# Kernel tuning notes

Hardware: AMD Instinct MI355X
Metric: run time of the kernel (lower is better)

The kernel has to match this reference:

```python
import jax, jax.numpy as jnp
import numpy as np

DIM = 256; QK = 256; HEADS = 8; TOPK = 2; WV = 2; WH = 2
SCALE = QK ** -0.5


def setup_inputs() -> dict:
    key = jax.random.key(0)
    ks = jax.random.split(key, 6)
    x = jax.random.normal(ks[0], (4, DIM, 64, 64), jnp.float32)
    Wqkv = jax.random.normal(ks[1], (DIM, 2 * QK + DIM), jnp.float32) * 0.02
    bqkv = jnp.zeros((2 * QK + DIM,), jnp.float32)
    Wo = jax.random.normal(ks[2], (DIM, DIM), jnp.float32) * 0.02
    bo = jnp.zeros((DIM,), jnp.float32)
    lepe_w = jax.random.normal(ks[3], (3, 3, 1, DIM), jnp.float32) * 0.1  # HWIO depthwise
    lepe_b = jnp.zeros((DIM,), jnp.float32)
    return {"x": x, "Wqkv": Wqkv, "bqkv": bqkv, "Wo": Wo, "bo": bo,
            "lepe_w": lepe_w, "lepe_b": lepe_b}


def _dwconv(x, w, b):
    # depthwise 3x3 conv, NHWC
    y = jax.lax.conv_general_dilated(x, w, (1, 1), 'SAME',
                                     dimension_numbers=('NHWC', 'HWIO', 'NHWC'),
                                     feature_group_count=x.shape[-1])
    return y + b


def _branch(win, Wqkv, bqkv, lepe_w, lepe_b, to_image):
    n, p2, h, w, _ = win.shape
    w2 = h * w
    qkv = win @ Wqkv + bqkv
    q = qkv[..., :QK]
    kv = qkv[..., QK:]                                  # [n,p2,h,w,QK+DIM]
    q_pix = q.reshape(n, p2, w2, QK)
    kv_pix = kv.reshape(n, p2, w2, QK + DIM)            # identity kv_down
    # region routing (detached in original)
    q_win = jax.lax.stop_gradient(q).mean((2, 3))       # [n,p2,QK]
    k_win = jax.lax.stop_gradient(kv[..., :QK]).mean((2, 3))
    logit = jnp.einsum('npc,nqc->npq', q_win * SCALE, k_win)
    _, r_idx = jax.lax.top_k(logit, TOPK)               # [n,p2,TOPK]
    # gather selected KV windows (mul_weight='none')
    kv_sel = jax.vmap(lambda kvb, idxb: kvb[idxb])(kv_pix, r_idx)  # [n,p2,k,w2,ckv]
    k_sel = kv_sel[..., :QK].reshape(n, p2, TOPK * w2, HEADS, QK // HEADS)
    v_sel = kv_sel[..., QK:].reshape(n, p2, TOPK * w2, HEADS, DIM // HEADS)
    qh = q_pix.reshape(n, p2, w2, HEADS, QK // HEADS)
    attn = jax.nn.softmax(jnp.einsum('npqhd,npkhd->nphqk', qh * SCALE, k_sel), axis=-1)
    out = jnp.einsum('nphqk,npkhd->npqhd', attn, v_sel).reshape(n, p2, h, w, DIM)
    lepe = _dwconv(to_image(kv[..., QK:]), lepe_w, lepe_b)
    return to_image(out) + lepe


def reference(x, Wqkv, bqkv, Wo, bo, lepe_w, lepe_b):
    xh = x.transpose(0, 2, 3, 1)                        # NHWC
    N, H, W, C = xh.shape
    v_win, h_win = H // WV, W // WH
    # vertical branch: horizontal strips of height WV, full width
    vm = xh.reshape(N, v_win, WV, W, C)
    # horizontal branch: vertical strips of width WH, full height
    hm = xh.reshape(N, H, h_win, WH, C).transpose(0, 2, 1, 3, 4)
    img_v = lambda a: a.reshape(N, H, W, a.shape[-1])
    img_h = lambda a: a.transpose(0, 2, 1, 3, 4).reshape(N, H, W, a.shape[-1])
    o1 = _branch(vm, Wqkv, bqkv, lepe_w, lepe_b, img_v)
    o2 = _branch(hm, Wqkv, bqkv, lepe_w, lepe_b, img_h)
    out = (o1 @ Wo + bo) + (o2 @ Wo + bo)
    return out.transpose(0, 3, 1, 2)                    # back to NCHW
```

## Files before the change

kernel.cpp:

```cpp
#include <hip/hip_runtime.h>
#include <hip/hip_bf16.h>
#include <math.h>

#define NBATCH 4
#define HW     4096
#define NPIX   16384
#define SCALE  0.0625f
#define QLOG2E (0.0625f * 1.44269504088896340736f)

typedef __attribute__((ext_vector_type(8))) short bf16x8;
typedef __attribute__((ext_vector_type(4))) float f32x4;

__device__ __forceinline__ int pixmap(int b, int n, int p, int pos){
  return (b == 0) ? (n*HW + p*128 + pos)
                  : (n*HW + (pos >> 1)*64 + (p << 1) + (pos & 1));
}

__device__ __forceinline__ ushort f2b(float x){
  __hip_bfloat16 h = __float2bfloat16(x);
  return *reinterpret_cast<ushort*>(&h);
}
__device__ __forceinline__ float b2f(ushort u){
  __hip_bfloat16 h = *reinterpret_cast<__hip_bfloat16*>(&u);
  return __bfloat162float(h);
}
__device__ __forceinline__ uint pk2t(float a, float b){
  return (__float_as_uint(a) >> 16) | (__float_as_uint(b) & 0xFFFF0000u);
}

__global__ __launch_bounds__(256) void k_xt(
    const float* __restrict__ x, ushort* __restrict__ Xb,
    float* __restrict__ pb0, float* __restrict__ pb1)
{
  __shared__ float T[32][257];
  const int n = blockIdx.y, blk = blockIdx.x, hw0 = blk * 32;
  const int tid = threadIdx.x;
  const int hl = tid & 31, cg = tid >> 5;
  #pragma unroll 8
  for(int i = 0; i < 32; i++){
    const int c = i*8 + cg;
    T[hl][c] = x[((size_t)(n*256 + c))*4096 + hw0 + hl];
  }
  __syncthreads();
  const int c0 = (tid & 31)*8, pbr = tid >> 5;
  #pragma unroll
  for(int i = 0; i < 4; i++){
    const int p = pbr + 8*i;
    union { bf16x8 v; ushort u[8]; } U;
    #pragma unroll
    for(int j = 0; j < 8; j++) U.u[j] = f2b(T[p][c0 + j]);
    *(bf16x8*)(Xb + ((size_t)(n*HW + hw0 + p))*256 + c0) = U.v;
  }
  const int c = tid;
  float s0 = 0.f;
  float* p1 = pb1 + (((size_t)n*128 + blk)*16)*256 + c;
  #pragma unroll
  for(int j = 0; j < 16; j++){
    const float pj = T[2*j][c] + T[2*j+1][c];
    p1[(size_t)j*256] = pj;
    s0 += pj;
  }
  pb0[((size_t)n*128 + blk)*256 + c] = s0;
}

__global__ __launch_bounds__(256) void k_xred(
    const float* __restrict__ pb0, const float* __restrict__ pb1,
    float* __restrict__ xwin)
{
  const int p = blockIdx.x;
  const int n = blockIdx.y;
  const int c = threadIdx.x;
  float s = 0.f;
  #pragma unroll
  for(int i = 0; i < 4; i++)
    s += pb0[((size_t)n*128 + 4*p + i)*256 + c];
  xwin[((size_t)((0*NBATCH + n)*32 + p))*256 + c] = s * (1.f/128.f);
  const int half = p >> 4, j = p & 15;
  float s1 = 0.f;
  for(int h = 0; h < 64; h++)
    s1 += pb1[(((size_t)n*128 + 2*h + half)*16 + j)*256 + c];
  xwin[((size_t)((1*NBATCH + n)*32 + p))*256 + c] = s1 * (1.f/128.f);
}

__global__ __launch_bounds__(256) void k_wprep(
    const float* __restrict__ Wqkv, const float* __restrict__ Wo,
    ushort* __restrict__ Wt, ushort* __restrict__ WoT)
{
  const int o = blockIdx.x, t = threadIdx.x;
  if(o < 768){
    Wt[(size_t)o*256 + t] = f2b(Wqkv[(size_t)t*768 + o]);
  } else {
    const int c = o - 768;
    WoT[(size_t)c*256 + t] = f2b(Wo[(size_t)t*256 + c]);
  }
}

__global__ __launch_bounds__(256) void k_qkv_mfma(
    const ushort* __restrict__ Xb, const ushort* __restrict__ Wt,
    const float* __restrict__ bqkv, ushort* __restrict__ QKVb,
    ushort* __restrict__ Vt)
{
  const int tid = threadIdx.x;
  const int l = tid & 63, w = tid >> 6;
  const int wr = w >> 1, wc = w & 1;
  const int q16 = l & 15, g = l >> 4;
  const int row0 = blockIdx.x*128 + wr*64;
  const int col0 = blockIdx.y*128 + wc*64;

  f32x4 acc[4][4];
  #pragma unroll
  for(int i = 0; i < 4; i++)
    #pragma unroll
    for(int j = 0; j < 4; j++) acc[i][j] = (f32x4){0,0,0,0};

  const ushort* Ab = Xb + (size_t)(row0 + q16)*256 + 8*g;
  const ushort* Bb = Wt + (size_t)(col0 + q16)*256 + 8*g;

  #pragma unroll
  for(int ks = 0; ks < 8; ks++){
    const int k0 = ks*32;
    bf16x8 a[4], b[4];
    #pragma unroll
    for(int i = 0; i < 4; i++) a[i] = *(const bf16x8*)(Ab + (size_t)(16*i)*256 + k0);
    #pragma unroll
    for(int j = 0; j < 4; j++) b[j] = *(const bf16x8*)(Bb + (size_t)(16*j)*256 + k0);
    #pragma unroll
    for(int i = 0; i < 4; i++)
      #pragma unroll
      for(int j = 0; j < 4; j++)
        acc[i][j] = __builtin_amdgcn_mfma_f32_16x16x32_bf16(a[i], b[j], acc[i][j], 0, 0, 0);
  }

  const int n = row0 >> 12, hwb = row0 & 4095;
  #pragma unroll
  for(int j = 0; j < 4; j++){
    const int col = col0 + 16*j + q16;
    const float bias = bqkv[col];
    const float sc = (col < 256) ? QLOG2E : 1.f;
    #pragma unroll
    for(int i = 0; i < 4; i++){
      ushort4 u;
      u.x = f2b((acc[i][j][0] + bias) * sc);
      u.y = f2b((acc[i][j][1] + bias) * sc);
      u.z = f2b((acc[i][j][2] + bias) * sc);
      u.w = f2b((acc[i][j][3] + bias) * sc);
      const int row = row0 + 16*i + 4*g;
      QKVb[(size_t)(row+0)*768 + col] = u.x;
      QKVb[(size_t)(row+1)*768 + col] = u.y;
      QKVb[(size_t)(row+2)*768 + col] = u.z;
      QKVb[(size_t)(row+3)*768 + col] = u.w;
      if(col >= 512){
        *(ushort4*)&Vt[((size_t)(n*256 + col - 512))*4096 + hwb + 16*i + 4*g] = u;
      }
    }
  }
}

__global__ __launch_bounds__(256) void k_win_gemm(
    const float* __restrict__ xwin, const float* __restrict__ Wqkv,
    const float* __restrict__ bqkv, float* __restrict__ qwin, float* __restrict__ kwin)
{
  __shared__ float xs[256];
  const int row = blockIdx.x;
  const int tid = threadIdx.x;
  xs[tid] = xwin[(size_t)row*256 + tid];
  __syncthreads();
  #pragma unroll
  for(int half = 0; half < 2; half++){
    const int col = half*256 + tid;
    float s = 0.f;
    for(int k = 0; k < 256; k++) s += xs[k] * Wqkv[(size_t)k*768 + col];
    s += bqkv[col];
    if(half == 0) qwin[(size_t)row*256 + tid] = s;
    else          kwin[(size_t)row*256 + tid] = s;
  }
}

__global__ __launch_bounds__(256) void k_logits_top2(
    const float* __restrict__ qwin, const float* __restrict__ kwin, int* __restrict__ ridx)
{
  const int n = blockIdx.x, b = blockIdx.y;
  __shared__ float lg[32][32];
  const int base = ((b*NBATCH + n)*32)*256;
  for(int t = threadIdx.x; t < 1024; t += 256){
    const int p = t >> 5, q = t & 31;
    const float* qp = qwin + base + p*256;
    const float* kq = kwin + base + q*256;
    float s = 0.f;
    for(int c = 0; c < 256; c++) s += qp[c]*kq[c];
    lg[p][q] = s * SCALE;
  }
  __syncthreads();
  if(threadIdx.x < 32){
    const int p = threadIdx.x;
    float m0 = -INFINITY; int i0 = 0;
    for(int q = 0; q < 32; q++){ const float v = lg[p][q]; if(v > m0){ m0 = v; i0 = q; } }
    float m1 = -INFINITY; int i1 = 0;
    for(int q = 0; q < 32; q++){ if(q == i0) continue; const float v = lg[p][q]; if(v > m1){ m1 = v; i1 = q; } }
    const int o = ((b*NBATCH + n)*32 + p)*2;
    ridx[o] = i0; ridx[o+1] = i1;
  }
}

struct KVFrag { bf16x8 kf0, kf1, vf0, vf1; };

__device__ __forceinline__ KVFrag load_kv(
    const ushort* __restrict__ QKVb, const ushort* __restrict__ Vt,
    int b, int n, int wsel, int posb, int hd, int q16, int g)
{
  KVFrag f;
  const int kp0 = pixmap(b, n, wsel, posb + q16);
  f.kf0 = *(const bf16x8*)(QKVb + (size_t)kp0*768 + 256 + hd*32 + 8*g);
  const int kp1 = pixmap(b, n, wsel, posb + 16 + q16);
  f.kf1 = *(const bf16x8*)(QKVb + (size_t)kp1*768 + 256 + hd*32 + 8*g);
  if(b == 0){
    const ushort* base = Vt + ((size_t)(n*256 + hd*32 + q16))*4096 + wsel*128 + posb + 4*g;
    union { bf16x8 v; ushort4 h[2]; } U0, U1;
    U0.h[0] = *(const ushort4*)(base);
    U0.h[1] = *(const ushort4*)(base + 16);
    U1.h[0] = *(const ushort4*)(base + (size_t)16*4096);
    U1.h[1] = *(const ushort4*)(base + (size_t)16*4096 + 16);
    f.vf0 = U0.v; f.vf1 = U1.v;
  } else {
    const int h0 = (posb + 4*g) >> 1;
    const ushort* base = Vt + ((size_t)(n*256 + hd*32 + q16))*4096 + 2*wsel;
    union { bf16x8 v; uint u[4]; } U0, U1;
    U0.u[0] = *(const uint*)(base + (h0    )*64);
    U0.u[1] = *(const uint*)(base + (h0 + 1)*64);
    U0.u[2] = *(const uint*)(base + (h0 + 8)*64);
    U0.u[3] = *(const uint*)(base + (h0 + 9)*64);
    const ushort* base1 = base + (size_t)16*4096;
    U1.u[0] = *(const uint*)(base1 + (h0    )*64);
    U1.u[1] = *(const uint*)(base1 + (h0 + 1)*64);
    U1.u[2] = *(const uint*)(base1 + (h0 + 8)*64);
    U1.u[3] = *(const uint*)(base1 + (h0 + 9)*64);
    f.vf0 = U0.v; f.vf1 = U1.v;
  }
  return f;
}

__global__ __launch_bounds__(256) void k_attn_mfma(
    const ushort* __restrict__ QKVb, const ushort* __restrict__ Vt,
    const int* __restrict__ ridx, ushort* __restrict__ Ob)
{
  int id = blockIdx.x*4 + (threadIdx.x >> 6);
  const int hd = id & 7;  id >>= 3;
  const int p  = id & 31; id >>= 5;
  const int n  = id & 3;  id >>= 2;
  const int b  = id;
  const int l = threadIdx.x & 63;
  const int q16 = l & 15, g = l >> 4;

  const int ro = ((b*NBATCH + n)*32 + p)*2;
  const int r0 = ridx[ro], r1 = ridx[ro+1];

  int qpix[8];
  bf16x8 qf[8];
  #pragma unroll
  for(int m = 0; m < 8; m++){
    qpix[m] = pixmap(b, n, p, m*16 + q16);
    qf[m] = *(const bf16x8*)(QKVb + (size_t)qpix[m]*768 + hd*32 + 8*g);
  }

  f32x4 acc0[8], acc1[8];
  float rs[8];
  #pragma unroll
  for(int m = 0; m < 8; m++){
    acc0[m] = (f32x4){0,0,0,0}; acc1[m] = (f32x4){0,0,0,0}; rs[m] = 0.f;
  }

  #define COMPUTE(F)                                                            \
    __builtin_amdgcn_s_setprio(1);                                              \
    _Pragma("unroll")                                                           \
    for(int m = 0; m < 8; m++){                                                 \
      const f32x4 z = {0,0,0,0};                                                \
      f32x4 s0 = __builtin_amdgcn_mfma_f32_16x16x32_bf16((F).kf0, qf[m], z, 0, 0, 0); \
      f32x4 s1 = __builtin_amdgcn_mfma_f32_16x16x32_bf16((F).kf1, qf[m], z, 0, 0, 0); \
      const float e00 = exp2f(s0[0]), e01 = exp2f(s0[1]), e02 = exp2f(s0[2]), e03 = exp2f(s0[3]); \
      const float e10 = exp2f(s1[0]), e11 = exp2f(s1[1]), e12 = exp2f(s1[2]), e13 = exp2f(s1[3]); \
      rs[m] += ((e00+e01)+(e02+e03)) + ((e10+e11)+(e12+e13));                   \
      union { bf16x8 v; uint u[4]; } P;                                         \
      P.u[0] = pk2t(e00, e01);                                                  \
      P.u[1] = pk2t(e02, e03);                                                  \
      P.u[2] = pk2t(e10, e11);                                                  \
      P.u[3] = pk2t(e12, e13);                                                  \
      acc0[m] = __builtin_amdgcn_mfma_f32_16x16x32_bf16((F).vf0, P.v, acc0[m], 0, 0, 0); \
      acc1[m] = __builtin_amdgcn_mfma_f32_16x16x32_bf16((F).vf1, P.v, acc1[m], 0, 0, 0); \
    }                                                                           \
    __builtin_amdgcn_s_setprio(0);

  KVFrag fA = load_kv(QKVb, Vt, b, n, r0, 0, hd, q16, g);
  for(int cc = 0; cc < 8; cc += 2){
    const int w1 = (cc+1 < 4) ? r0 : r1;
    KVFrag fB = load_kv(QKVb, Vt, b, n, w1, (32*(cc+1)) & 127, hd, q16, g);
    COMPUTE(fA);
    if(cc + 2 < 8){
      const int w2 = (cc+2 < 4) ? r0 : r1;
      fA = load_kv(QKVb, Vt, b, n, w2, (32*(cc+2)) & 127, hd, q16, g);
    }
    COMPUTE(fB);
  }
  #undef COMPUTE

  #pragma unroll
  for(int m = 0; m < 8; m++){
    float r = rs[m];
    r += __shfl_xor(r, 16);
    r += __shfl_xor(r, 32);
    rs[m] = 1.f / r;
  }
  #pragma unroll
  for(int m = 0; m < 8; m++){
    ushort* op = Ob + ((size_t)b*NPIX + qpix[m])*256 + hd*32 + 4*g;
    const float iv = rs[m];
    ushort4 o0 = { f2b(acc0[m][0]*iv), f2b(acc0[m][1]*iv), f2b(acc0[m][2]*iv), f2b(acc0[m][3]*iv) };
    ushort4 o1 = { f2b(acc1[m][0]*iv), f2b(acc1[m][1]*iv), f2b(acc1[m][2]*iv), f2b(acc1[m][3]*iv) };
    *(ushort4*)op = o0;
    *(ushort4*)(op + 16) = o1;
  }
}

__global__ __launch_bounds__(256) void k_combine_lepe(
    const ushort* __restrict__ QKVb, const ushort* __restrict__ Ob0,
    const ushort* __restrict__ Ob1,
    const float* __restrict__ lw, const float* __restrict__ lb, ushort* __restrict__ Sb)
{
  const int pix = blockIdx.x;
  const int c = threadIdx.x;
  const int n = pix >> 12, rem = pix & 4095;
  const int h = rem >> 6, w = rem & 63;
  float conv = 0.f;
  #pragma unroll
  for(int kh = 0; kh < 3; kh++){
    const int hh = h + kh - 1;
    if(hh < 0 || hh >= 64) continue;
    #pragma unroll
    for(int kw = 0; kw < 3; kw++){
      const int wi = w + kw - 1;
      if(wi < 0 || wi >= 64) continue;
      const int np = (n*64 + hh)*64 + wi;
      conv += b2f(QKVb[(size_t)np*768 + 512 + c]) * lw[(kh*3 + kw)*256 + c];
    }
  }
  const size_t idx = (size_t)pix*256 + c;
  Sb[idx] = f2b(b2f(Ob0[idx]) + b2f(Ob1[idx]) + 2.f*(conv + lb[c]));
}

__global__ __launch_bounds__(256) void k_out_mfma(
    const ushort* __restrict__ Sb, const ushort* __restrict__ WoT,
    const float* __restrict__ bo, float* __restrict__ out)
{
  const int tid = threadIdx.x;
  const int l = tid & 63, w = tid >> 6;
  const int wr = w >> 1, wc = w & 1;
  const int q16 = l & 15, g = l >> 4;
  const int c0   = blockIdx.x*128 + wr*64;
  const int pix0 = blockIdx.y*128 + wc*64;
  const int n = pix0 >> 12, rem0 = pix0 & 4095;

  f32x4 acc[4][4];
  #pragma unroll
  for(int i = 0; i < 4; i++)
    #pragma unroll
    for(int j = 0; j < 4; j++) acc[i][j] = (f32x4){0,0,0,0};

  const ushort* Ab = WoT + (size_t)(c0 + q16)*256 + 8*g;
  const ushort* Bb = Sb  + (size_t)(pix0 + q16)*256 + 8*g;

  #pragma unroll
  for(int ks = 0; ks < 8; ks++){
    const int k0 = ks*32;
    bf16x8 a[4], b[4];
    #pragma unroll
    for(int i = 0; i < 4; i++) a[i] = *(const bf16x8*)(Ab + (size_t)(16*i)*256 + k0);
    #pragma unroll
    for(int j = 0; j < 4; j++) b[j] = *(const bf16x8*)(Bb + (size_t)(16*j)*256 + k0);
    #pragma unroll
    for(int i = 0; i < 4; i++)
      #pragma unroll
      for(int j = 0; j < 4; j++)
        acc[i][j] = __builtin_amdgcn_mfma_f32_16x16x32_bf16(a[i], b[j], acc[i][j], 0, 0, 0);
  }

  float* outn = out + (size_t)n*256*4096;
  #pragma unroll
  for(int i = 0; i < 4; i++){
    #pragma unroll
    for(int r = 0; r < 4; r++){
      const int c = c0 + 16*i + 4*g + r;
      const float bias = 2.f*bo[c];
      #pragma unroll
      for(int j = 0; j < 4; j++){
        const int rem = rem0 + 16*j + q16;
        outn[(size_t)c*4096 + rem] = acc[i][j][r] + bias;
      }
    }
  }
}

extern "C" void kernel_launch(void* const* d_in, const int* in_sizes, int n_in,
                              void* d_out, int out_size, void* d_ws, size_t ws_size,
                              hipStream_t stream)
{
  const float* x    = (const float*)d_in[0];
  const float* Wqkv = (const float*)d_in[1];
  const float* bqkv = (const float*)d_in[2];
  const float* Wo   = (const float*)d_in[3];
  const float* bo   = (const float*)d_in[4];
  const float* lw   = (const float*)d_in[5];
  const float* lb   = (const float*)d_in[6];
  float* out = (float*)d_out;

  char* w = (char*)d_ws;
  ushort* Xb   = (ushort*)w; w += (size_t)NPIX*256*2;
  ushort* Wt   = (ushort*)w; w += (size_t)768*256*2;
  ushort* WoT  = (ushort*)w; w += (size_t)256*256*2;
  ushort* QKVb = (ushort*)w; w += (size_t)NPIX*768*2;
  ushort* Vt   = (ushort*)w; w += (size_t)NPIX*256*2;
  ushort* Ob   = (ushort*)w; w += (size_t)2*NPIX*256*2;
  ushort* Sb   = (ushort*)w; w += (size_t)NPIX*256*2;
  float*  pb0  = (float*)w;  w += (size_t)NBATCH*128*256*4;
  float*  pb1  = (float*)w;  w += (size_t)NBATCH*128*16*256*4;
  float*  xwin = (float*)w;  w += (size_t)2*NBATCH*32*256*4;
  float*  qwin = (float*)w;  w += (size_t)2*NBATCH*32*256*4;
  float*  kwin = (float*)w;  w += (size_t)2*NBATCH*32*256*4;
  int*    ridx = (int*)w;    w += (size_t)2*NBATCH*32*2*4;

  ushort* Ob0 = Ob;
  ushort* Ob1 = Ob + (size_t)NPIX*256;

  k_xt          <<<dim3(128,NBATCH), 256, 0, stream>>>(x, Xb, pb0, pb1);
  k_xred        <<<dim3(32,NBATCH), 256, 0, stream>>>(pb0, pb1, xwin);
  k_wprep       <<<1024, 256, 0, stream>>>(Wqkv, Wo, Wt, WoT);
  k_qkv_mfma    <<<dim3(128,6), 256, 0, stream>>>(Xb, Wt, bqkv, QKVb, Vt);
  k_win_gemm    <<<256, 256, 0, stream>>>(xwin, Wqkv, bqkv, qwin, kwin);
  k_logits_top2 <<<dim3(NBATCH,2), 256, 0, stream>>>(qwin, kwin, ridx);
  k_attn_mfma   <<<512, 256, 0, stream>>>(QKVb, Vt, ridx, Ob);
  k_combine_lepe<<<NPIX, 256, 0, stream>>>(QKVb, Ob0, Ob1, lw, lb, Sb);
  k_out_mfma    <<<dim3(2,128), 256, 0, stream>>>(Sb, WoT, bo, out);
}
```

Baseline: 178.9 us.

## Split attention KV windows across wave pairs and combine partials via LDS

Each (branch, batch, window, head) attention task is now handled by two waves, each covering one of the two selected KV windows, instead of one wave covering both. Partial accumulators and row sums from the second wave are passed through shared memory and added by the first wave before normalizing and writing. The grid doubles to 1024 blocks to raise parallelism and cut per-wave serial latency. This adds an LDS buffer, a block barrier and redundant Q loads. Since exp2 is applied without a max subtraction, the two partials can be summed directly.

```diff
diff --git a/kernel.cpp b/kernel.cpp
--- a/kernel.cpp
+++ b/kernel.cpp
@@ -243,7 +243,10 @@
     const ushort* __restrict__ QKVb, const ushort* __restrict__ Vt,
     const int* __restrict__ ridx, ushort* __restrict__ Ob)
 {
-  int id = blockIdx.x*4 + (threadIdx.x >> 6);
+  __shared__ float comb[2][64][76];
+  const int wv = threadIdx.x >> 6;
+  const int pair = wv >> 1, half = wv & 1;
+  int id = blockIdx.x*2 + pair;
   const int hd = id & 7;  id >>= 3;
   const int p  = id & 31; id >>= 5;
   const int n  = id & 3;  id >>= 2;
@@ -252,7 +255,7 @@
   const int q16 = l & 15, g = l >> 4;
 
   const int ro = ((b*NBATCH + n)*32 + p)*2;
-  const int r0 = ridx[ro], r1 = ridx[ro+1];
+  const int wsel = ridx[ro + half];
 
   int qpix[8];
   bf16x8 qf[8];
@@ -289,34 +292,53 @@
     }                                                                           \
     __builtin_amdgcn_s_setprio(0);
 
-  KVFrag fA = load_kv(QKVb, Vt, b, n, r0, 0, hd, q16, g);
-  for(int cc = 0; cc < 8; cc += 2){
-    const int w1 = (cc+1 < 4) ? r0 : r1;
-    KVFrag fB = load_kv(QKVb, Vt, b, n, w1, (32*(cc+1)) & 127, hd, q16, g);
+  KVFrag fA = load_kv(QKVb, Vt, b, n, wsel, 0, hd, q16, g);
+  {
+    KVFrag fB = load_kv(QKVb, Vt, b, n, wsel, 32, hd, q16, g);
     COMPUTE(fA);
-    if(cc + 2 < 8){
-      const int w2 = (cc+2 < 4) ? r0 : r1;
-      fA = load_kv(QKVb, Vt, b, n, w2, (32*(cc+2)) & 127, hd, q16, g);
-    }
+    fA = load_kv(QKVb, Vt, b, n, wsel, 64, hd, q16, g);
     COMPUTE(fB);
+    fB = load_kv(QKVb, Vt, b, n, wsel, 96, hd, q16, g);
+    COMPUTE(fA);
+    COMPUTE(fB);
   }
   #undef COMPUTE
 
-  #pragma unroll
-  for(int m = 0; m < 8; m++){
-    float r = rs[m];
-    r += __shfl_xor(r, 16);
-    r += __shfl_xor(r, 32);
-    rs[m] = 1.f / r;
-  }
-  #pragma unroll
-  for(int m = 0; m < 8; m++){
-    ushort* op = Ob + ((size_t)b*NPIX + qpix[m])*256 + hd*32 + 4*g;
-    const float iv = rs[m];
-    ushort4 o0 = { f2b(acc0[m][0]*iv), f2b(acc0[m][1]*iv), f2b(acc0[m][2]*iv), f2b(acc0[m][3]*iv) };
-    ushort4 o1 = { f2b(acc1[m][0]*iv), f2b(acc1[m][1]*iv), f2b(acc1[m][2]*iv), f2b(acc1[m][3]*iv) };
-    *(ushort4*)op = o0;
-    *(ushort4*)(op + 16) = o1;
+  float* cb = &comb[pair][l][0];
+  if(half == 1){
+    #pragma unroll
+    for(int m = 0; m < 8; m++){
+      *(float4*)(cb + m*8)     = (float4){acc0[m][0], acc0[m][1], acc0[m][2], acc0[m][3]};
+      *(float4*)(cb + m*8 + 4) = (float4){acc1[m][0], acc1[m][1], acc1[m][2], acc1[m][3]};
+      cb[64 + m] = rs[m];
+    }
+  }
+  __syncthreads();
+  if(half == 0){
+    #pragma unroll
+    for(int m = 0; m < 8; m++){
+      const float4 a0 = *(const float4*)(cb + m*8);
+      const float4 a1 = *(const float4*)(cb + m*8 + 4);
+      acc0[m][0] += a0.x; acc0[m][1] += a0.y; acc0[m][2] += a0.z; acc0[m][3] += a0.w;
+      acc1[m][0] += a1.x; acc1[m][1] += a1.y; acc1[m][2] += a1.z; acc1[m][3] += a1.w;
+      rs[m] += cb[64 + m];
+    }
+    #pragma unroll
+    for(int m = 0; m < 8; m++){
+      float r = rs[m];
+      r += __shfl_xor(r, 16);
+      r += __shfl_xor(r, 32);
+      rs[m] = 1.f / r;
+    }
+    #pragma unroll
+    for(int m = 0; m < 8; m++){
+      ushort* op = Ob + ((size_t)b*NPIX + qpix[m])*256 + hd*32 + 4*g;
+      const float iv = rs[m];
+      ushort4 o0 = { f2b(acc0[m][0]*iv), f2b(acc0[m][1]*iv), f2b(acc0[m][2]*iv), f2b(acc0[m][3]*iv) };
+      ushort4 o1 = { f2b(acc1[m][0]*iv), f2b(acc1[m][1]*iv), f2b(acc1[m][2]*iv), f2b(acc1[m][3]*iv) };
+      *(ushort4*)op = o0;
+      *(ushort4*)(op + 16) = o1;
+    }
   }
 }
 
@@ -435,7 +457,7 @@
   k_qkv_mfma    <<<dim3(128,6), 256, 0, stream>>>(Xb, Wt, bqkv, QKVb, Vt);
   k_win_gemm    <<<256, 256, 0, stream>>>(xwin, Wqkv, bqkv, qwin, kwin);
   k_logits_top2 <<<dim3(NBATCH,2), 256, 0, stream>>>(qwin, kwin, ridx);
-  k_attn_mfma   <<<512, 256, 0, stream>>>(QKVb, Vt, ridx, Ob);
+  k_attn_mfma   <<<1024, 256, 0, stream>>>(QKVb, Vt, ridx, Ob);
   k_combine_lepe<<<NPIX, 256, 0, stream>>>(QKVb, Ob0, Ob1, lw, lb, Sb);
   k_out_mfma    <<<dim3(2,128), 256, 0, stream>>>(Sb, WoT, bo, out);
 }
```

New measurement: 198.8 us. +11.1%, slower.
